# Performance work log

Hardware: AMD Instinct MI355X
Metric: run time of the kernel (lower is better)

## Reference

```python
import jax, jax.numpy as jnp
import numpy as np

B, T, E, H = 4, 1024, 1024, 16
D = E // H  # head_dim = 64


def setup_inputs() -> dict:
    key = jax.random.key(0)
    ks = jax.random.split(key, 6)
    s = 0.02  # realistic init scale for stable softmax
    return {
        "hidden_states": jax.random.normal(ks[0], (B, T, E), jnp.float32),
        "attention_mask": jnp.zeros((B, 1, T, T), jnp.float32),
        "Wq": jax.random.normal(ks[1], (E, E), jnp.float32) * s,
        "bq": jnp.zeros((E,), jnp.float32),
        "Wk": jax.random.normal(ks[2], (E, E), jnp.float32) * s,
        "bk": jnp.zeros((E,), jnp.float32),
        "Wv": jax.random.normal(ks[3], (E, E), jnp.float32) * s,
        "bv": jnp.zeros((E,), jnp.float32),
        "Wo": jax.random.normal(ks[4], (E, E), jnp.float32) * s,
        "bo": jnp.zeros((E,), jnp.float32),
    }


def reference(hidden_states, attention_mask, Wq, bq, Wk, bk, Wv, bv, Wo, bo):
    b, t, e = hidden_states.shape
    scaling = jnp.asarray(D, hidden_states.dtype) ** -0.5
    # q_proj weights/bias are pre-scaled in the module; equivalent to scaling q output
    q = (hidden_states @ Wq.T + bq) * scaling      # [B,T,E]
    k = hidden_states @ Wk.T + bk                   # self-attention path (no cache)
    v = hidden_states @ Wv.T + bv
    q = q.reshape(b, t, H, D)
    k = k.reshape(b, t, H, D)
    v = v.reshape(b, t, H, D)
    # bmm(q, k^T): [B,H,T,S] score matrix (materialized, as in the original)
    scores = jnp.einsum("bthd,bshd->bhts", q, k) + attention_mask
    probs = jax.nn.softmax(scores, axis=-1)
    ctx = jnp.einsum("bhts,bshd->bthd", probs, v).reshape(b, t, e)
    return ctx @ Wo.T + bo
```

## Files before the change

### kernel.cpp

```cpp
#include <hip/hip_runtime.h>
#include <math.h>

#define BB 4
#define TT 1024
#define EE 1024
#define HH 16
#define DD 64
#define KDIM 1024
#define N_HS (4096 * 1024)
#define N_W  (1024 * 1024)
#define NQKV (BB * HH * TT * DD)
#define NMASK (BB * TT * TT)

typedef _Float16 f16x8 __attribute__((ext_vector_type(8)));
typedef float    f32x4 __attribute__((ext_vector_type(4)));

__device__ __forceinline__ unsigned short f2h(float x) {
    _Float16 h = (_Float16)x;
    return __builtin_bit_cast(unsigned short, h);
}
__device__ __forceinline__ void split_h(float x, unsigned short& hi, unsigned short& lo) {
    _Float16 h = (_Float16)x;
    hi = __builtin_bit_cast(unsigned short, h);
    lo = f2h(x - (float)h);
}

__device__ __forceinline__ void gload16(const void* g, void* l) {
    __builtin_amdgcn_global_load_lds(
        (const __attribute__((address_space(1))) void*)g,
        (__attribute__((address_space(3))) void*)l, 16, 0, 0);
}

__global__ __launch_bounds__(256)
void split_kernel(const float* __restrict__ hs,
                  const float* __restrict__ Wq, const float* __restrict__ Wk,
                  const float* __restrict__ Wv, const float* __restrict__ Wo,
                  const float* __restrict__ maskp,
                  unsigned short* __restrict__ ws,
                  unsigned short* __restrict__ maskh)
{
    const int u = blockIdx.x * 256 + threadIdx.x;
    const float* src;
    unsigned short* dst;
    if (u < (N_HS / 4)) {
        src = hs + (size_t)u * 4;
        dst = ws + (size_t)u * 4;
    } else if (u < (N_HS / 4) + N_W) {
        int v = u - N_HS / 4;
        int wsel = v >> 18;
        int wo   = v & 0x3FFFF;
        const float* Wsrc = (wsel == 0) ? Wq : (wsel == 1) ? Wk : (wsel == 2) ? Wv : Wo;
        src = Wsrc + (size_t)wo * 4;
        dst = ws + (size_t)N_HS + (size_t)wsel * N_W + (size_t)wo * 4;
    } else {
        int v = u - (N_HS / 4) - N_W;
        src = maskp + (size_t)v * 4;
        dst = maskh + (size_t)v * 4;
    }
    float4 x = *(const float4*)src;
    ushort4 h4;
    h4.x = f2h(x.x); h4.y = f2h(x.y); h4.z = f2h(x.z); h4.w = f2h(x.w);
    *(ushort4*)dst = h4;
}

__global__ __launch_bounds__(256)
void qkv_kernel(const unsigned short* __restrict__ hsp,
                const unsigned short* __restrict__ wqp,
                const float* __restrict__ bq, const float* __restrict__ bk,
                const float* __restrict__ bv,
                unsigned short* __restrict__ qkvb)
{
    __shared__ unsigned short Ah[128 * 32], Bh[128 * 32];

    const int widx  = blockIdx.x >> 3;
    const int nbase = (blockIdx.x & 7) * 128;
    const int mbase = blockIdx.y * 128;
    const unsigned short* Wp = wqp + (size_t)widx * N_W;
    const float* bias = (widx == 0) ? bq : (widx == 1) ? bk : bv;
    const float scale = (widx == 0) ? 0.125f : 1.0f;

    const int tid  = threadIdx.x;
    const int w    = tid >> 6;
    const int lane = tid & 63;
    const int quad = lane >> 4;
    const int l16  = lane & 15;
    const int wm   = (w >> 1) * 64;
    const int wn   = (w & 1) * 64;

    f32x4 acc[4][4];
#pragma unroll
    for (int i = 0; i < 4; i++)
#pragma unroll
        for (int j = 0; j < 4; j++) acc[i][j] = (f32x4)0.f;

#pragma unroll 1
    for (int kt = 0; kt < KDIM; kt += 32) {
        __syncthreads();
#pragma unroll
        for (int i = 0; i < 2; i++) {
            int u = tid + i * 256;
            int r = u >> 2, c = u & 3;
            int q = c ^ ((r >> 1) & 3);
            gload16(hsp + (size_t)(mbase + r) * KDIM + kt + q * 8, &Ah[u * 8]);
            gload16(Wp  + (size_t)(nbase + r) * KDIM + kt + q * 8, &Bh[u * 8]);
        }
        __syncthreads();

        f16x8 af[4], bfr[4];
#pragma unroll
        for (int i = 0; i < 4; i++) {
            int r = wm + i * 16 + l16;
            af[i] = *(const f16x8*)&Ah[(r * 4 + (quad ^ ((r >> 1) & 3))) * 8];
        }
#pragma unroll
        for (int j = 0; j < 4; j++) {
            int r = wn + j * 16 + l16;
            bfr[j] = *(const f16x8*)&Bh[(r * 4 + (quad ^ ((r >> 1) & 3))) * 8];
        }
#pragma unroll
        for (int i = 0; i < 4; i++)
#pragma unroll
            for (int j = 0; j < 4; j++)
                acc[i][j] = __builtin_amdgcn_mfma_f32_16x16x32_f16(af[i], bfr[j], acc[i][j], 0, 0, 0);
    }

    if (widx == 2) {
        unsigned short* vtp = qkvb + 2 * (size_t)NQKV;
#pragma unroll
        for (int j = 0; j < 4; j++) {
            int n = nbase + wn + j * 16 + l16;
            int h = n >> 6, d = n & 63;
            float bj = bias[n];
#pragma unroll
            for (int i = 0; i < 4; i++) {
                int m = mbase + wm + i * 16 + quad * 4;
                int b = m >> 10, t0 = m & 1023;
                ushort4 pk;
                pk.x = f2h(acc[i][j][0] + bj);
                pk.y = f2h(acc[i][j][1] + bj);
                pk.z = f2h(acc[i][j][2] + bj);
                pk.w = f2h(acc[i][j][3] + bj);
                *(ushort4*)(vtp + ((size_t)(b * HH + h) * DD + d) * TT + t0) = pk;
            }
        }
    } else {
        unsigned short* dst = qkvb + (size_t)widx * NQKV;
#pragma unroll
        for (int j = 0; j < 4; j++) {
            int n = nbase + wn + j * 16 + l16;
            int h = n >> 6, d = n & 63;
            float bj = bias[n];
#pragma unroll
            for (int i = 0; i < 4; i++)
#pragma unroll
                for (int rr = 0; rr < 4; rr++) {
                    int m = mbase + wm + i * 16 + quad * 4 + rr;
                    int b = m >> 10, t = m & 1023;
                    dst[(((size_t)(b * HH + h) * TT + t) * DD + d)] =
                        f2h((acc[i][j][rr] + bj) * scale);
                }
        }
    }
}

__global__ __launch_bounds__(256)
void outproj_kernel(const unsigned short* __restrict__ ctxh,
                    const unsigned short* __restrict__ ctxl,
                    const unsigned short* __restrict__ wop,
                    const float* __restrict__ bo, float* __restrict__ out)
{
    __shared__ unsigned short Ach[64 * 32], Acl[64 * 32], Bh[128 * 32];

    const int nbase = blockIdx.x * 128;
    const int mbase = blockIdx.y * 64;

    const int tid  = threadIdx.x;
    const int w    = tid >> 6;
    const int lane = tid & 63;
    const int quad = lane >> 4;
    const int l16  = lane & 15;
    const int wm   = (w >> 1) * 32;
    const int wn   = (w & 1) * 64;

    f32x4 acc[2][4];
#pragma unroll
    for (int i = 0; i < 2; i++)
#pragma unroll
        for (int j = 0; j < 4; j++) acc[i][j] = (f32x4)0.f;

#pragma unroll 1
    for (int kt = 0; kt < KDIM; kt += 32) {
        __syncthreads();
        {
            int r = tid >> 2, c = tid & 3;
            int q = c ^ ((r >> 1) & 3);
            size_t ga = (size_t)(mbase + r) * KDIM + kt + q * 8;
            gload16(ctxh + ga, &Ach[tid * 8]);
            gload16(ctxl + ga, &Acl[tid * 8]);
        }
#pragma unroll
        for (int i = 0; i < 2; i++) {
            int u = tid + i * 256;
            int r = u >> 2, c = u & 3;
            int q = c ^ ((r >> 1) & 3);
            gload16(wop + (size_t)(nbase + r) * KDIM + kt + q * 8, &Bh[u * 8]);
        }
        __syncthreads();

        f16x8 ah[2], al[2], bfr[4];
#pragma unroll
        for (int i = 0; i < 2; i++) {
            int r = wm + i * 16 + l16;
            int slot = (r * 4 + (quad ^ ((r >> 1) & 3))) * 8;
            ah[i] = *(const f16x8*)&Ach[slot];
            al[i] = *(const f16x8*)&Acl[slot];
        }
#pragma unroll
        for (int j = 0; j < 4; j++) {
            int r = wn + j * 16 + l16;
            bfr[j] = *(const f16x8*)&Bh[(r * 4 + (quad ^ ((r >> 1) & 3))) * 8];
        }
#pragma unroll
        for (int i = 0; i < 2; i++)
#pragma unroll
            for (int j = 0; j < 4; j++) {
                acc[i][j] = __builtin_amdgcn_mfma_f32_16x16x32_f16(ah[i], bfr[j], acc[i][j], 0, 0, 0);
                acc[i][j] = __builtin_amdgcn_mfma_f32_16x16x32_f16(al[i], bfr[j], acc[i][j], 0, 0, 0);
            }
    }

#pragma unroll
    for (int j = 0; j < 4; j++) {
        int n = nbase + wn + j * 16 + l16;
        float bj = bo[n];
#pragma unroll
        for (int i = 0; i < 2; i++)
#pragma unroll
            for (int rr = 0; rr < 4; rr++) {
                int m = mbase + wm + i * 16 + quad * 4 + rr;
                out[(size_t)m * EE + n] = acc[i][j][rr] + bj;
            }
    }
}

__global__ __launch_bounds__(128)
void attn_kernel(const unsigned short* __restrict__ qp_, const unsigned short* __restrict__ kp_,
                 const unsigned short* __restrict__ vtp_,
                 const unsigned short* __restrict__ maskh,
                 unsigned short* __restrict__ ctxh, unsigned short* __restrict__ ctxl)
{
    __shared__ unsigned short Ks[64 * 64];
    __shared__ unsigned short Vt[64 * 64];
    __shared__ unsigned short Ps[32 * 64];

    const int bh = blockIdx.x;
    const int b  = bh >> 4;
    const int h  = bh & 15;
    const int m0 = blockIdx.y * 32;
    const size_t hoff = (size_t)bh * TT * DD;
    const unsigned short* qhp = qp_ + hoff;
    const unsigned short* khp = kp_ + hoff;
    const unsigned short* vtp = vtp_ + hoff;
    const _Float16* mb = (const _Float16*)(maskh + (size_t)b * TT * TT);

    const int tid  = threadIdx.x;
    const int w    = tid >> 6;
    const int lane = tid & 63;
    const int quad = lane >> 4;
    const int l16  = lane & 15;

    f16x8 ones;
#pragma unroll
    for (int j = 0; j < 8; j++) ones[j] = (_Float16)1.0f;

    f16x8 qf[2];
#pragma unroll
    for (int s = 0; s < 2; s++)
        qf[s] = *(const f16x8*)(qhp + (size_t)(m0 + w * 16 + l16) * DD + s * 32 + quad * 8);

    f32x4 o[4], lacc = (f32x4)0.f;
    float m_q = -INFINITY;
#pragma unroll
    for (int t = 0; t < 4; t++) o[t] = (f32x4)0.f;

#pragma unroll 1
    for (int n0 = 0; n0 < TT; n0 += 64) {
        _Float16 mreg[4][4];
#pragma unroll
        for (int t = 0; t < 4; t++)
#pragma unroll
            for (int r = 0; r < 4; r++)
                mreg[t][r] = mb[(size_t)(m0 + w * 16 + quad * 4 + r) * TT + n0 + 16 * t + l16];

        __syncthreads();
#pragma unroll
        for (int i = 0; i < 4; i++) {
            int u = tid + i * 128;
            int r = u >> 3, cp = u & 7;
            int c = cp ^ (r & 7);
            gload16(khp + (size_t)(n0 + r) * DD + c * 8, &Ks[u * 8]);
            gload16(vtp + (size_t)r * TT + n0 + c * 8,   &Vt[u * 8]);
        }
        __syncthreads();

        f32x4 st[4];
#pragma unroll
        for (int t = 0; t < 4; t++) st[t] = (f32x4)0.f;
#pragma unroll
        for (int s = 0; s < 2; s++)
#pragma unroll
            for (int t = 0; t < 4; t++) {
                int R = 16 * t + l16;
                const f16x8 kf = *(const f16x8*)&Ks[(R * 8 + ((s * 4 + quad) ^ (R & 7))) * 8];
                st[t] = __builtin_amdgcn_mfma_f32_16x16x32_f16(qf[s], kf, st[t], 0, 0, 0);
            }
#pragma unroll
        for (int t = 0; t < 4; t++)
#pragma unroll
            for (int r = 0; r < 4; r++)
                st[t][r] += (float)mreg[t][r];

        float rm = st[0][0];
#pragma unroll
        for (int t = 0; t < 4; t++)
#pragma unroll
            for (int r = 0; r < 4; r++) rm = fmaxf(rm, st[t][r]);
#pragma unroll
        for (int mky = 1; mky < 16; mky <<= 1)
            rm = fmaxf(rm, __shfl_xor(rm, mky));
        float mnew  = fmaxf(m_q, rm);
        float alpha = __expf(m_q - mnew);
        m_q = mnew;

#pragma unroll
        for (int t = 0; t < 4; t++)
#pragma unroll
            for (int r = 0; r < 4; r++)
                st[t][r] = __expf(st[t][r] - m_q);
#pragma unroll
        for (int t = 0; t < 4; t++)
#pragma unroll
            for (int r = 0; r < 4; r++)
                o[t][r] *= alpha;
        lacc *= alpha;

#pragma unroll
        for (int t = 0; t < 4; t++)
#pragma unroll
            for (int r = 0; r < 4; r++) {
                int R = w * 16 + quad * 4 + r;
                int j = 16 * t + l16;
                Ps[R * 64 + (((j >> 3) ^ (R & 7)) * 8) + (j & 7)] = f2h(st[t][r]);
            }

#pragma unroll
        for (int s = 0; s < 2; s++) {
            int Rr = w * 16 + l16;
            const f16x8 pf = *(const f16x8*)&Ps[Rr * 64 + (((s * 4 + quad) ^ (Rr & 7)) * 8)];
            lacc = __builtin_amdgcn_mfma_f32_16x16x32_f16(pf, ones, lacc, 0, 0, 0);
#pragma unroll
            for (int t = 0; t < 4; t++) {
                int R = 16 * t + l16;
                const f16x8 vf = *(const f16x8*)&Vt[(R * 8 + ((s * 4 + quad) ^ (R & 7))) * 8];
                o[t] = __builtin_amdgcn_mfma_f32_16x16x32_f16(pf, vf, o[t], 0, 0, 0);
            }
        }
    }

#pragma unroll
    for (int r = 0; r < 4; r++) {
        float inv = 1.0f / lacc[r];
        int m = m0 + w * 16 + quad * 4 + r;
#pragma unroll
        for (int t = 0; t < 4; t++) {
            float val = o[t][r] * inv;
            unsigned short hi, lo;
            split_h(val, hi, lo);
            size_t off = (size_t)(b * TT + m) * EE + h * DD + 16 * t + l16;
            ctxh[off] = hi;
            ctxl[off] = lo;
        }
    }
}

extern "C" void kernel_launch(void* const* d_in, const int* in_sizes, int n_in,
                              void* d_out, int out_size, void* d_ws, size_t ws_size,
                              hipStream_t stream)
{
    const float* hs   = (const float*)d_in[0];
    const float* mask = (const float*)d_in[1];
    const float* Wq   = (const float*)d_in[2];
    const float* bq   = (const float*)d_in[3];
    const float* Wk   = (const float*)d_in[4];
    const float* bk   = (const float*)d_in[5];
    const float* Wv   = (const float*)d_in[6];
    const float* bv   = (const float*)d_in[7];
    const float* Wo   = (const float*)d_in[8];
    const float* bo   = (const float*)d_in[9];
    float* out = (float*)d_out;

    unsigned short* ws    = (unsigned short*)d_ws;
    unsigned short* hsp   = ws;
    unsigned short* wqp   = ws + (size_t)N_HS;
    unsigned short* wop   = wqp + 3 * (size_t)N_W;
    unsigned short* qkvb  = wqp + 4 * (size_t)N_W;
    unsigned short* qp    = qkvb;
    unsigned short* kp    = qp + (size_t)NQKV;
    unsigned short* vtp   = kp + (size_t)NQKV;
    unsigned short* ctxl  = vtp + (size_t)NQKV;
    unsigned short* maskh = ctxl + (size_t)N_HS;
    unsigned short* ctxh  = ws;

    split_kernel<<<12288, 256, 0, stream>>>(hs, Wq, Wk, Wv, Wo, mask, ws, maskh);
    qkv_kernel<<<dim3(24, 32), 256, 0, stream>>>(hsp, wqp, bq, bk, bv, qkvb);
    attn_kernel<<<dim3(BB * HH, TT / 32), 128, 0, stream>>>(qp, kp, vtp, maskh, ctxh, ctxl);
    outproj_kernel<<<dim3(8, 64), 256, 0, stream>>>(ctxh, ctxl, wop, bo, out);
}
```

Before: 244.3 us.

## Transpose score tile to keep probabilities in registers and add V transpose kernel

The attention kernel now computes S^T (K as the A operand), so the exponentiated probabilities already sit in the B-operand layout of the 16x16x16 MFMA. This removes the shared-memory round trip for P and the ones-vector MFMA that computed row sums; row sums are now accumulated in registers and reduced with shuffles. The mask tile is staged through LDS with 16-byte loads instead of scattered scalar half loads, and the context output goes through LDS so global writes are coalesced. The V transpose moves out of the QKV epilogue into a separate LDS-tiled kernel, which adds a launch and an extra buffer in the workspace.

```diff
diff --git a/kernel.cpp b/kernel.cpp
--- a/kernel.cpp
+++ b/kernel.cpp
@@ -13,6 +13,7 @@
 #define NMASK (BB * TT * TT)
 
 typedef _Float16 f16x8 __attribute__((ext_vector_type(8)));
+typedef _Float16 f16x4 __attribute__((ext_vector_type(4)));
 typedef float    f32x4 __attribute__((ext_vector_type(4)));
 
 __device__ __forceinline__ unsigned short f2h(float x) {
@@ -77,6 +78,7 @@
     const int mbase = blockIdx.y * 128;
     const unsigned short* Wp = wqp + (size_t)widx * N_W;
     const float* bias = (widx == 0) ? bq : (widx == 1) ? bk : bv;
+    unsigned short* dst = qkvb + (size_t)widx * NQKV;
     const float scale = (widx == 0) ? 0.125f : 1.0f;
 
     const int tid  = threadIdx.x;
@@ -124,42 +126,54 @@
                 acc[i][j] = __builtin_amdgcn_mfma_f32_16x16x32_f16(af[i], bfr[j], acc[i][j], 0, 0, 0);
     }
 
-    if (widx == 2) {
-        unsigned short* vtp = qkvb + 2 * (size_t)NQKV;
-#pragma unroll
-        for (int j = 0; j < 4; j++) {
-            int n = nbase + wn + j * 16 + l16;
-            int h = n >> 6, d = n & 63;
-            float bj = bias[n];
-#pragma unroll
-            for (int i = 0; i < 4; i++) {
-                int m = mbase + wm + i * 16 + quad * 4;
-                int b = m >> 10, t0 = m & 1023;
-                ushort4 pk;
-                pk.x = f2h(acc[i][j][0] + bj);
-                pk.y = f2h(acc[i][j][1] + bj);
-                pk.z = f2h(acc[i][j][2] + bj);
-                pk.w = f2h(acc[i][j][3] + bj);
-                *(ushort4*)(vtp + ((size_t)(b * HH + h) * DD + d) * TT + t0) = pk;
-            }
-        }
-    } else {
-        unsigned short* dst = qkvb + (size_t)widx * NQKV;
-#pragma unroll
-        for (int j = 0; j < 4; j++) {
-            int n = nbase + wn + j * 16 + l16;
-            int h = n >> 6, d = n & 63;
-            float bj = bias[n];
-#pragma unroll
-            for (int i = 0; i < 4; i++)
-#pragma unroll
-                for (int rr = 0; rr < 4; rr++) {
-                    int m = mbase + wm + i * 16 + quad * 4 + rr;
-                    int b = m >> 10, t = m & 1023;
-                    dst[(((size_t)(b * HH + h) * TT + t) * DD + d)] =
-                        f2h((acc[i][j][rr] + bj) * scale);
-                }
-        }
+#pragma unroll
+    for (int j = 0; j < 4; j++) {
+        int n = nbase + wn + j * 16 + l16;
+        int h = n >> 6, d = n & 63;
+        float bj = bias[n];
+#pragma unroll
+        for (int i = 0; i < 4; i++)
+#pragma unroll
+            for (int rr = 0; rr < 4; rr++) {
+                int m = mbase + wm + i * 16 + quad * 4 + rr;
+                int b = m >> 10, t = m & 1023;
+                dst[(((size_t)(b * HH + h) * TT + t) * DD + d)] =
+                    f2h((acc[i][j][rr] + bj) * scale);
+            }
+    }
+}
+
+__global__ __launch_bounds__(256)
+void vtrans_kernel(const unsigned short* __restrict__ vp,
+                   unsigned short* __restrict__ vtp)
+{
+    __shared__ unsigned short Ts[64 * 72];
+    const int bh = blockIdx.y;
+    const int t0 = blockIdx.x * 64;
+    const unsigned short* src = vp  + (size_t)bh * TT * DD + (size_t)t0 * DD;
+    unsigned short*       dst = vtp + (size_t)bh * DD * TT + t0;
+    const int tid = threadIdx.x;
+
+#pragma unroll
+    for (int i = 0; i < 2; i++) {
+        int id = tid + i * 256;
+        int r = id >> 3, c = id & 7;
+        *(uint4*)&Ts[r * 72 + c * 8] = *(const uint4*)(src + (size_t)r * DD + c * 8);
+    }
+    __syncthreads();
+#pragma unroll
+    for (int i = 0; i < 2; i++) {
+        int id = tid + i * 256;
+        int d = id >> 3, c = id & 7;
+        unsigned short tmp[8];
+#pragma unroll
+        for (int j = 0; j < 8; j++) tmp[j] = Ts[(c * 8 + j) * 72 + d];
+        uint4 o;
+        o.x = (unsigned int)tmp[0] | ((unsigned int)tmp[1] << 16);
+        o.y = (unsigned int)tmp[2] | ((unsigned int)tmp[3] << 16);
+        o.z = (unsigned int)tmp[4] | ((unsigned int)tmp[5] << 16);
+        o.w = (unsigned int)tmp[6] | ((unsigned int)tmp[7] << 16);
+        *(uint4*)(dst + (size_t)d * TT + c * 8) = o;
     }
 }
 
@@ -251,7 +265,7 @@
 {
     __shared__ unsigned short Ks[64 * 64];
     __shared__ unsigned short Vt[64 * 64];
-    __shared__ unsigned short Ps[32 * 64];
+    __shared__ unsigned short Ms[32 * 72];
 
     const int bh = blockIdx.x;
     const int b  = bh >> 4;
@@ -261,7 +275,7 @@
     const unsigned short* qhp = qp_ + hoff;
     const unsigned short* khp = kp_ + hoff;
     const unsigned short* vtp = vtp_ + hoff;
-    const _Float16* mb = (const _Float16*)(maskh + (size_t)b * TT * TT);
+    const unsigned short* mb  = maskh + (size_t)b * TT * TT;
 
     const int tid  = threadIdx.x;
     const int w    = tid >> 6;
@@ -269,29 +283,18 @@
     const int quad = lane >> 4;
     const int l16  = lane & 15;
 
-    f16x8 ones;
-#pragma unroll
-    for (int j = 0; j < 8; j++) ones[j] = (_Float16)1.0f;
-
     f16x8 qf[2];
 #pragma unroll
     for (int s = 0; s < 2; s++)
         qf[s] = *(const f16x8*)(qhp + (size_t)(m0 + w * 16 + l16) * DD + s * 32 + quad * 8);
 
-    f32x4 o[4], lacc = (f32x4)0.f;
-    float m_q = -INFINITY;
-#pragma unroll
-    for (int t = 0; t < 4; t++) o[t] = (f32x4)0.f;
+    f32x4 o[4];
+#pragma unroll
+    for (int u = 0; u < 4; u++) o[u] = (f32x4)0.f;
+    float m_run = -INFINITY, lacc = 0.f;
 
 #pragma unroll 1
     for (int n0 = 0; n0 < TT; n0 += 64) {
-        _Float16 mreg[4][4];
-#pragma unroll
-        for (int t = 0; t < 4; t++)
-#pragma unroll
-            for (int r = 0; r < 4; r++)
-                mreg[t][r] = mb[(size_t)(m0 + w * 16 + quad * 4 + r) * TT + n0 + 16 * t + l16];
-
         __syncthreads();
 #pragma unroll
         for (int i = 0; i < 4; i++) {
@@ -301,6 +304,13 @@
             gload16(khp + (size_t)(n0 + r) * DD + c * 8, &Ks[u * 8]);
             gload16(vtp + (size_t)r * TT + n0 + c * 8,   &Vt[u * 8]);
         }
+#pragma unroll
+        for (int i = 0; i < 2; i++) {
+            int cch = tid * 2 + i;
+            int row = cch >> 3, c8 = cch & 7;
+            uint4 mv = *(const uint4*)(mb + (size_t)(m0 + row) * TT + n0 + c8 * 8);
+            *(uint4*)&Ms[row * 72 + c8 * 8] = mv;
+        }
         __syncthreads();
 
         f32x4 st[4];
@@ -312,74 +322,92 @@
             for (int t = 0; t < 4; t++) {
                 int R = 16 * t + l16;
                 const f16x8 kf = *(const f16x8*)&Ks[(R * 8 + ((s * 4 + quad) ^ (R & 7))) * 8];
-                st[t] = __builtin_amdgcn_mfma_f32_16x16x32_f16(qf[s], kf, st[t], 0, 0, 0);
-            }
+                st[t] = __builtin_amdgcn_mfma_f32_16x16x32_f16(kf, qf[s], st[t], 0, 0, 0);
+            }
+#pragma unroll
+        for (int t = 0; t < 4; t++) {
+            f16x4 mk = *(const f16x4*)&Ms[(w * 16 + l16) * 72 + 16 * t + quad * 4];
+#pragma unroll
+            for (int r = 0; r < 4; r++)
+                st[t][r] += (float)mk[r];
+        }
+
+        float rm = st[0][0];
 #pragma unroll
         for (int t = 0; t < 4; t++)
 #pragma unroll
+            for (int r = 0; r < 4; r++) rm = fmaxf(rm, st[t][r]);
+        rm = fmaxf(rm, __shfl_xor(rm, 16));
+        rm = fmaxf(rm, __shfl_xor(rm, 32));
+        float mnew  = fmaxf(m_run, rm);
+        float alpha = __expf(m_run - mnew);
+        m_run = mnew;
+
+        float ls = 0.f;
+#pragma unroll
+        for (int t = 0; t < 4; t++)
+#pragma unroll
+            for (int r = 0; r < 4; r++) {
+                float p = __expf(st[t][r] - m_run);
+                st[t][r] = p;
+                ls += p;
+            }
+        lacc = lacc * alpha + ls;
+#pragma unroll
+        for (int u = 0; u < 4; u++)
+#pragma unroll
             for (int r = 0; r < 4; r++)
-                st[t][r] += (float)mreg[t][r];
-
-        float rm = st[0][0];
+                o[u][r] *= alpha;
+
+        f16x4 pf[4];
 #pragma unroll
         for (int t = 0; t < 4; t++)
 #pragma unroll
-            for (int r = 0; r < 4; r++) rm = fmaxf(rm, st[t][r]);
-#pragma unroll
-        for (int mky = 1; mky < 16; mky <<= 1)
-            rm = fmaxf(rm, __shfl_xor(rm, mky));
-        float mnew  = fmaxf(m_q, rm);
-        float alpha = __expf(m_q - mnew);
-        m_q = mnew;
+            for (int r = 0; r < 4; r++)
+                pf[t][r] = (_Float16)st[t][r];
 
 #pragma unroll
         for (int t = 0; t < 4; t++)
 #pragma unroll
-            for (int r = 0; r < 4; r++)
-                st[t][r] = __expf(st[t][r] - m_q);
-#pragma unroll
-        for (int t = 0; t < 4; t++)
-#pragma unroll
-            for (int r = 0; r < 4; r++)
-                o[t][r] *= alpha;
-        lacc *= alpha;
-
-#pragma unroll
-        for (int t = 0; t < 4; t++)
-#pragma unroll
-            for (int r = 0; r < 4; r++) {
-                int R = w * 16 + quad * 4 + r;
-                int j = 16 * t + l16;
-                Ps[R * 64 + (((j >> 3) ^ (R & 7)) * 8) + (j & 7)] = f2h(st[t][r]);
-            }
-
-#pragma unroll
-        for (int s = 0; s < 2; s++) {
-            int Rr = w * 16 + l16;
-            const f16x8 pf = *(const f16x8*)&Ps[Rr * 64 + (((s * 4 + quad) ^ (Rr & 7)) * 8)];
-            lacc = __builtin_amdgcn_mfma_f32_16x16x32_f16(pf, ones, lacc, 0, 0, 0);
-#pragma unroll
-            for (int t = 0; t < 4; t++) {
-                int R = 16 * t + l16;
-                const f16x8 vf = *(const f16x8*)&Vt[(R * 8 + ((s * 4 + quad) ^ (R & 7))) * 8];
-                o[t] = __builtin_amdgcn_mfma_f32_16x16x32_f16(pf, vf, o[t], 0, 0, 0);
-            }
-        }
-    }
-
-#pragma unroll
-    for (int r = 0; r < 4; r++) {
-        float inv = 1.0f / lacc[r];
-        int m = m0 + w * 16 + quad * 4 + r;
-#pragma unroll
-        for (int t = 0; t < 4; t++) {
-            float val = o[t][r] * inv;
+            for (int u = 0; u < 4; u++) {
+                int r_ = 16 * u + l16;
+                int lc = 2 * t + (quad >> 1);
+                int pc = lc ^ (r_ & 7);
+                const f16x4 vf = *(const f16x4*)&Vt[r_ * 64 + pc * 8 + (quad & 1) * 4];
+                o[u] = __builtin_amdgcn_mfma_f32_16x16x16f16(vf, pf[t], o[u], 0, 0, 0);
+            }
+    }
+
+    lacc += __shfl_xor(lacc, 16);
+    lacc += __shfl_xor(lacc, 32);
+    const float inv = 1.0f / lacc;
+
+    __syncthreads();
+#pragma unroll
+    for (int u = 0; u < 4; u++)
+#pragma unroll
+        for (int r = 0; r < 4; r++) {
+            float val = o[u][r] * inv;
             unsigned short hi, lo;
             split_h(val, hi, lo);
-            size_t off = (size_t)(b * TT + m) * EE + h * DD + 16 * t + l16;
-            ctxh[off] = hi;
-            ctxl[off] = lo;
-        }
+            int mloc = w * 16 + l16;
+            int d    = 16 * u + quad * 4 + r;
+            Ks[mloc * 72 + d] = hi;
+            Vt[mloc * 72 + d] = lo;
+        }
+    __syncthreads();
+    {
+        int row = tid >> 2;
+        int c16 = (tid & 3) * 16;
+        size_t base = ((size_t)(b * TT + m0 + row)) * EE + h * DD + c16;
+        uint4 h0 = *(const uint4*)&Ks[row * 72 + c16];
+        uint4 h1 = *(const uint4*)&Ks[row * 72 + c16 + 8];
+        *(uint4*)(ctxh + base)     = h0;
+        *(uint4*)(ctxh + base + 8) = h1;
+        uint4 l0 = *(const uint4*)&Vt[row * 72 + c16];
+        uint4 l1 = *(const uint4*)&Vt[row * 72 + c16 + 8];
+        *(uint4*)(ctxl + base)     = l0;
+        *(uint4*)(ctxl + base + 8) = l1;
     }
 }
 
@@ -406,13 +434,15 @@
     unsigned short* qkvb  = wqp + 4 * (size_t)N_W;
     unsigned short* qp    = qkvb;
     unsigned short* kp    = qp + (size_t)NQKV;
-    unsigned short* vtp   = kp + (size_t)NQKV;
+    unsigned short* vp    = kp + (size_t)NQKV;
+    unsigned short* vtp   = vp + (size_t)NQKV;
     unsigned short* ctxl  = vtp + (size_t)NQKV;
     unsigned short* maskh = ctxl + (size_t)N_HS;
     unsigned short* ctxh  = ws;
 
     split_kernel<<<12288, 256, 0, stream>>>(hs, Wq, Wk, Wv, Wo, mask, ws, maskh);
     qkv_kernel<<<dim3(24, 32), 256, 0, stream>>>(hsp, wqp, bq, bk, bv, qkvb);
+    vtrans_kernel<<<dim3(TT / 64, BB * HH), 256, 0, stream>>>(vp, vtp);
     attn_kernel<<<dim3(BB * HH, TT / 32), 128, 0, stream>>>(qp, kp, vtp, maskh, ctxh, ctxl);
     outproj_kernel<<<dim3(8, 64), 256, 0, stream>>>(ctxh, ctxl, wop, bo, out);
 }
```

Measured after the change: 235.6 us. 1.04x faster.
